# Optimization experiments

Hardware: AMD Instinct MI355X
Metric: run time of the kernel (lower is better)

## Reference

```python
import jax, jax.numpy as jnp
import numpy as np

NUM_HEADS = 16
HIDDEN = 1024
HEAD_DIM = HIDDEN // NUM_HEADS


def setup_inputs() -> dict:
    key = jax.random.key(0)
    ks = jax.random.split(key, 9)
    B, S, D = 2, 2048, HIDDEN
    s = 1.0 / np.sqrt(D)
    return {
        "x": jax.random.normal(ks[0], (B, S, D), dtype=jnp.float32),
        "Wq": jax.random.normal(ks[1], (D, D), dtype=jnp.float32) * s,
        "bq": jnp.zeros((D,), dtype=jnp.float32),
        "Wk": jax.random.normal(ks[2], (D, D), dtype=jnp.float32) * s,
        "bk": jnp.zeros((D,), dtype=jnp.float32),
        "Wv": jax.random.normal(ks[3], (D, D), dtype=jnp.float32) * s,
        "bv": jnp.zeros((D,), dtype=jnp.float32),
        "Wo": jax.random.normal(ks[4], (D, D), dtype=jnp.float32) * s,
        "bo": jnp.zeros((D,), dtype=jnp.float32),
    }


def reference(x, Wq, bq, Wk, bk, Wv, bv, Wo, bo):
    B, S, D = x.shape
    H, Hd = NUM_HEADS, HEAD_DIM
    # projections -> [B, H, S, Hd]
    def proj(W, b):
        return (x @ W + b).reshape(B, S, H, Hd).transpose(0, 2, 1, 3)
    q = proj(Wq, bq)
    k = proj(Wk, bk)
    v = proj(Wv, bv)
    scores = jnp.einsum('bhqd,bhkd->bhqk', q, k) / jnp.sqrt(jnp.float32(Hd))
    p_attn = jax.nn.softmax(scores, axis=-1)  # dropout = identity (eval)
    ctx = jnp.einsum('bhqk,bhkd->bhqd', p_attn, v)
    attn_mean = jnp.mean(p_attn, axis=1)  # [B, S, S]
    out = ctx.transpose(0, 2, 1, 3).reshape(B, S, D) @ Wo + bo
    return out, attn_mean
```

## Files before the change

### kernel.cpp

```cpp
#include <hip/hip_runtime.h>
#include <math.h>

#define NUM_HEADS 16
#define HEAD_DIM  64
#define HIDDEN    1024
#define BATCH     2
#define SEQ       2048

#define QSCALE 0.1803368801111204f

typedef short bf16x8 __attribute__((ext_vector_type(8)));
typedef short short4v __attribute__((ext_vector_type(4)));
typedef float f32x4 __attribute__((ext_vector_type(4)));

#if __has_builtin(__builtin_amdgcn_exp2f)
#define EXP2F __builtin_amdgcn_exp2f
#else
#define EXP2F exp2f
#endif

#define ACQB(N) do { asm volatile("s_waitcnt vmcnt(" #N ")" ::: "memory"); \
                     __builtin_amdgcn_s_barrier(); } while (0)
#define RELB()  do { asm volatile("s_waitcnt lgkmcnt(0)" ::: "memory");   \
                     __builtin_amdgcn_sched_barrier(0);                    \
                     __builtin_amdgcn_s_barrier(); } while (0)
#define BARR()  do { asm volatile("s_waitcnt vmcnt(0) lgkmcnt(0)" ::: "memory"); \
                     __builtin_amdgcn_sched_barrier(0);                    \
                     __builtin_amdgcn_s_barrier(); } while (0)

__device__ __forceinline__ short f2bf(float f) {
    union { float f; unsigned int u; } x; x.f = f;
    unsigned int r = x.u + 0x7fffu + ((x.u >> 16) & 1u);
    return (short)(r >> 16);
}

__device__ __forceinline__ unsigned int pack_bf16_trunc(float lo, float hi) {
    return __builtin_amdgcn_perm(__float_as_uint(hi), __float_as_uint(lo), 0x07060302u);
}

__device__ __forceinline__ void async16(const void* g, void* l) {
    __builtin_amdgcn_global_load_lds(
        (const __attribute__((address_space(1))) void*)g,
        (__attribute__((address_space(3))) void*)l, 16, 0, 0);
}

__global__ __launch_bounds__(256)
void prep_kernel(const float* __restrict__ x,
                 const float* __restrict__ Wq, const float* __restrict__ Wk,
                 const float* __restrict__ Wv, const float* __restrict__ Wo,
                 short* __restrict__ xb, short* __restrict__ Wt4)
{
    __shared__ float t[64][65];
    const int tid = threadIdx.x;
    const int bid = blockIdx.x;
    if (bid < 4096) {
        size_t i = ((size_t)bid * 256 + tid) * 4;
        float4 v = *(const float4*)&x[i];
        short4v o;
        o.x = f2bf(v.x); o.y = f2bf(v.y); o.z = f2bf(v.z); o.w = f2bf(v.w);
        *(short4v*)&xb[i] = o;
        return;
    }
    const int tb = bid - 4096;
    const int z  = tb >> 8;
    const int cx = tb & 15, cy = (tb >> 4) & 15;
    const float* W = (z == 0) ? Wq : (z == 1) ? Wk : (z == 2) ? Wv : Wo;
    short* dst = Wt4 + (size_t)z * HIDDEN * HIDDEN;
    const int c0 = cx * 64;
    const int r0 = cy * 64;
    const int cl = tid & 63, rw = tid >> 6;
    #pragma unroll
    for (int p = 0; p < 16; ++p) {
        int row = p * 4 + rw;
        t[row][cl] = W[(size_t)(r0 + row) * HIDDEN + c0 + cl];
    }
    __syncthreads();
    #pragma unroll
    for (int p = 0; p < 16; ++p) {
        int orow = p * 4 + rw;
        dst[(size_t)(c0 + orow) * HIDDEN + r0 + cl] = f2bf(t[cl][orow]);
    }
}

__global__ __launch_bounds__(256)
void qkv_proj_kernel(const short* __restrict__ xb, const short* __restrict__ Wt4,
                     const float* __restrict__ bq, const float* __restrict__ bk,
                     const float* __restrict__ bv,
                     short* __restrict__ Qb, short* __restrict__ Kb,
                     short* __restrict__ Vt)
{
    __shared__ short ldsA[128 * 64];
    __shared__ short ldsB[128 * 64];
    const int tid = threadIdx.x;
    const int lane = tid & 63, w = tid >> 6;
    const int l = lane & 15, q = lane >> 4;
    const int lin = blockIdx.y * 8 + blockIdx.x;
    const int cid = (lin & 7) * 32 + (lin >> 3);
    const int n0 = (cid & 7) * 128;
    const int m0 = (cid >> 3) * 128;
    const int z  = blockIdx.z;
    const short* Wt = Wt4 + (size_t)z * HIDDEN * HIDDEN;
    const int wm = (w >> 1) * 64, wn = (w & 1) * 64;
    const int sw = l & 7;

    const short* pa[4]; const short* pb[4]; int ldst[4];
    #pragma unroll
    for (int hh = 0; hh < 4; ++hh) {
        int c = hh * 256 + tid;
        int row = c >> 3;
        int kcg = (c & 7) ^ (row & 7);
        pa[hh] = xb + (size_t)(m0 + row) * HIDDEN + kcg * 8;
        pb[hh] = Wt + (size_t)(n0 + row) * HIDDEN + kcg * 8;
        ldst[hh] = c * 8;
    }

    f32x4 acc[4][4];
    #pragma unroll
    for (int i = 0; i < 4; ++i)
        #pragma unroll
        for (int j = 0; j < 4; ++j)
            acc[i][j] = (f32x4){0.f, 0.f, 0.f, 0.f};

    auto STG = [&]() {
        #pragma unroll
        for (int hh = 0; hh < 4; ++hh) {
            async16(pa[hh], &ldsA[ldst[hh]]);
            async16(pb[hh], &ldsB[ldst[hh]]);
            pa[hh] += 64; pb[hh] += 64;
        }
    };

    STG();
    ACQB(0);
    for (int t = 0; t < 16; ++t) {
        bf16x8 af[4][2], bfr[4][2];
        #pragma unroll
        for (int kk = 0; kk < 2; ++kk) {
            const int cc = ((4 * kk + q) ^ sw) * 8;
            #pragma unroll
            for (int i = 0; i < 4; ++i)
                af[i][kk] = *(const bf16x8*)&ldsA[(wm + 16 * i + l) * 64 + cc];
            #pragma unroll
            for (int j = 0; j < 4; ++j)
                bfr[j][kk] = *(const bf16x8*)&ldsB[(wn + 16 * j + l) * 64 + cc];
        }
        RELB();
        if (t < 15) STG();
        __builtin_amdgcn_s_setprio(1);
        #pragma unroll
        for (int kk = 0; kk < 2; ++kk)
            #pragma unroll
            for (int i = 0; i < 4; ++i)
                #pragma unroll
                for (int j = 0; j < 4; ++j)
                    acc[i][j] = __builtin_amdgcn_mfma_f32_16x16x32_bf16(
                        af[i][kk], bfr[j][kk], acc[i][j], 0, 0, 0);
        __builtin_amdgcn_s_setprio(0);
        if (t < 15) ACQB(0);
    }

    const float* bias = (z == 0) ? bq : (z == 1) ? bk : bv;
    const float sc = (z == 0) ? QSCALE : 1.0f;
    if (z < 2) {
        short* Ob = (z == 0) ? Qb : Kb;
        #pragma unroll
        for (int j = 0; j < 4; ++j) {
            int n = n0 + wn + 16 * j + l;
            float bval = bias[n];
            int h = n >> 6, hd = n & 63;
            #pragma unroll
            for (int i = 0; i < 4; ++i) {
                #pragma unroll
                for (int reg = 0; reg < 4; ++reg) {
                    int m = m0 + wm + 16 * i + 4 * q + reg;
                    int b_ = m >> 11, s = m & 2047;
                    Ob[(((size_t)(b_ * NUM_HEADS + h) * SEQ) + s) * HEAD_DIM + hd] =
                        f2bf((acc[i][j][reg] + bval) * sc);
                }
            }
        }
    } else {
        #pragma unroll
        for (int j = 0; j < 4; ++j) {
            int n = n0 + wn + 16 * j + l;
            float bval = bias[n];
            int h = n >> 6, hd = n & 63;
            #pragma unroll
            for (int i = 0; i < 4; ++i) {
                int mb = m0 + wm + 16 * i + 4 * q;
                int b_ = mb >> 11, s = mb & 2047;
                short4v pk;
                #pragma unroll
                for (int reg = 0; reg < 4; ++reg)
                    pk[reg] = f2bf(acc[i][j][reg] + bval);
                *(short4v*)&Vt[(((size_t)(b_ * NUM_HEADS + h) * HEAD_DIM) + hd) * SEQ + s] = pk;
            }
        }
    }
}

__global__ __launch_bounds__(512, 4)
void flash_kernel(const short* __restrict__ Qb, const short* __restrict__ Kb,
                  const short* __restrict__ Vt, short* __restrict__ Cb,
                  float* __restrict__ Lb)
{
    __shared__ __align__(16) char fsm[35840];
    short (*Ks)[64 * 64] = (short (*)[64 * 64])fsm;
    short (*Vs)[64 * 64] = (short (*)[64 * 64])(fsm + 16384);
    float (*Xch)[64][35] = (float (*)[64][35])fsm;

    const int tid = threadIdx.x, lane = tid & 63, w = tid >> 6;
    const int l = lane & 15, q = lane >> 4;
    const int qg = w & 3;
    const int kh = w >> 2;
    const int q0 = blockIdx.x * 128;
    const int Q0 = q0 + qg * 32;
    const int h = blockIdx.y, b = blockIdx.z;
    const size_t base  = (size_t)(b * NUM_HEADS + h) * SEQ * HEAD_DIM;
    const size_t vbase = (size_t)(b * NUM_HEADS + h) * HEAD_DIM * SEQ;

    bf16x8 bq[2][2];
    #pragma unroll
    for (int u = 0; u < 2; ++u)
        #pragma unroll
        for (int ks = 0; ks < 2; ++ks)
            bq[u][ks] = *(const bf16x8*)(Qb + base +
                (size_t)(Q0 + 16 * u + l) * HEAD_DIM + 32 * ks + 8 * q);

    const int c = tid;
    const int row = c >> 3;
    const int g = ((c & 7) ^ (row & 7)) * 8;
    const short* kp = Kb + base + (size_t)row * HEAD_DIM + g;
    const short* vp = Vt + vbase + (size_t)row * SEQ + g;

    const int sw = l & 7;
    int kaddr[2];
    #pragma unroll
    for (int ks = 0; ks < 2; ++ks)
        kaddr[ks] = (32 * kh + l) * 64 + ((4 * ks + q) ^ sw) * 8;
    const int vc0 = 4 * kh + (q >> 1);
    const int vaddr0 = l * 64 + ((vc0      ^ sw) * 8) + 4 * (q & 1);
    const int vaddr1 = l * 64 + (((vc0 + 2) ^ sw) * 8) + 4 * (q & 1);

    f32x4 ctx[2][4];
    #pragma unroll
    for (int u = 0; u < 2; ++u)
        #pragma unroll
        for (int m = 0; m < 4; ++m) ctx[u][m] = (f32x4){0.f, 0.f, 0.f, 0.f};
    float l_part[2] = {0.f, 0.f};

    auto STG = [&](int buf) {
        async16(kp, &Ks[buf][c * 8]);
        async16(vp, &Vs[buf][c * 8]);
        kp += 64 * HEAD_DIM;
        vp += 64;
    };
    auto CMP = [&](int buf) {
        f32x4 st[2][2];
        #pragma unroll
        for (int u = 0; u < 2; ++u)
            #pragma unroll
            for (int t = 0; t < 2; ++t) st[u][t] = (f32x4){0.f, 0.f, 0.f, 0.f};
        __builtin_amdgcn_s_setprio(1);
        #pragma unroll
        for (int ks = 0; ks < 2; ++ks) {
            #pragma unroll
            for (int t = 0; t < 2; ++t) {
                bf16x8 ak = *(const bf16x8*)&Ks[buf][kaddr[ks] + t * 1024];
                st[0][t] = __builtin_amdgcn_mfma_f32_16x16x32_bf16(ak, bq[0][ks], st[0][t], 0, 0, 0);
                st[1][t] = __builtin_amdgcn_mfma_f32_16x16x32_bf16(ak, bq[1][ks], st[1][t], 0, 0, 0);
            }
        }
        __builtin_amdgcn_s_setprio(0);
        union { unsigned int u32[4]; bf16x8 v; } bp[2];
        #pragma unroll
        for (int u = 0; u < 2; ++u) {
            #pragma unroll
            for (int t = 0; t < 2; ++t) {
                float p0 = EXP2F(st[u][t][0]);
                float p1 = EXP2F(st[u][t][1]);
                float p2 = EXP2F(st[u][t][2]);
                float p3 = EXP2F(st[u][t][3]);
                l_part[u] += (p0 + p1) + (p2 + p3);
                bp[u].u32[2 * t]     = pack_bf16_trunc(p0, p1);
                bp[u].u32[2 * t + 1] = pack_bf16_trunc(p2, p3);
            }
        }
        __builtin_amdgcn_s_setprio(1);
        #pragma unroll
        for (int m = 0; m < 4; ++m) {
            short4v g0 = *(const short4v*)&Vs[buf][vaddr0 + m * 1024];
            short4v g1 = *(const short4v*)&Vs[buf][vaddr1 + m * 1024];
            bf16x8 av = __builtin_shufflevector(g0, g1, 0, 1, 2, 3, 4, 5, 6, 7);
            ctx[0][m] = __builtin_amdgcn_mfma_f32_16x16x32_bf16(av, bp[0].v, ctx[0][m], 0, 0, 0);
            ctx[1][m] = __builtin_amdgcn_mfma_f32_16x16x32_bf16(av, bp[1].v, ctx[1][m], 0, 0, 0);
        }
        __builtin_amdgcn_s_setprio(0);
    };

    STG(0);
    for (int t = 0; t < 32; ++t) {
        BARR();
        if (t < 31) STG((t + 1) & 1);
        CMP(t & 1);
    }

    __syncthreads();

    if (kh == 1) {
        float* dst = &Xch[qg][lane][0];
        #pragma unroll
        for (int u = 0; u < 2; ++u)
            #pragma unroll
            for (int m = 0; m < 4; ++m)
                #pragma unroll
                for (int r = 0; r < 4; ++r)
                    dst[u * 16 + m * 4 + r] = ctx[u][m][r];
        dst[32] = l_part[0];
        dst[33] = l_part[1];
    }
    __syncthreads();
    if (kh == 0) {
        const float* src = &Xch[qg][lane][0];
        #pragma unroll
        for (int u = 0; u < 2; ++u)
            #pragma unroll
            for (int m = 0; m < 4; ++m)
                #pragma unroll
                for (int r = 0; r < 4; ++r)
                    ctx[u][m][r] += src[u * 16 + m * 4 + r];

        #pragma unroll
        for (int u = 0; u < 2; ++u) {
            float rs = l_part[u] + src[32 + u];
            rs += __shfl_xor(rs, 16);
            rs += __shfl_xor(rs, 32);
            float inv_l = 1.0f / rs;
            int s = Q0 + 16 * u + l;
            #pragma unroll
            for (int t = 0; t < 4; ++t) {
                short4v pk;
                #pragma unroll
                for (int reg = 0; reg < 4; ++reg)
                    pk[reg] = f2bf(ctx[u][t][reg] * inv_l);
                *(short4v*)&Cb[(((size_t)(b * NUM_HEADS + h) * SEQ) + s) * HEAD_DIM + 16 * t + 4 * q] = pk;
            }
            if (q == 0)
                Lb[(size_t)(b * NUM_HEADS + h) * SEQ + s] = inv_l;
        }
    }
}

__global__ __launch_bounds__(256)
void tail_kernel(const short* __restrict__ Cb, const short* __restrict__ Wot,
                 const float* __restrict__ bo, float* __restrict__ out,
                 const short* __restrict__ Qb, const short* __restrict__ Kb,
                 const float* __restrict__ Lb, float* __restrict__ amean)
{
    __shared__ __align__(16) short smem[26624];
    const int tid = threadIdx.x, lane = tid & 63, w = tid >> 6;
    const int l = lane & 15, q = lane >> 4;
    const int sw = l & 7;
    const int bid = blockIdx.x;
    const int r3 = bid % 3, g3 = bid / 3;

    if (r3 == 2) {
        short (*ldsA)[64 * 64]  = (short (*)[64 * 64])smem;
        short (*ldsB)[128 * 64] = (short (*)[128 * 64])(smem + 8192);
        const int cid = (g3 & 7) * 64 + (g3 >> 3);
        const int n0 = (cid & 7) * 128;
        const int m0 = (cid >> 3) * 64;

        const short* pa[2]; const short* pb[4]; int lda[2], ldb[4];
        #pragma unroll
        for (int hh = 0; hh < 2; ++hh) {
            int cc = hh * 256 + tid;
            int rowc = cc >> 3;
            int kcg = (cc & 7) ^ (rowc & 7);
            int m = m0 + rowc;
            int b_ = m >> 11, s = m & 2047;
            pa[hh] = Cb + (((size_t)(b_ * NUM_HEADS) * SEQ) + s) * HEAD_DIM + kcg * 8;
            lda[hh] = cc * 8;
        }
        #pragma unroll
        for (int hh = 0; hh < 4; ++hh) {
            int cc = hh * 256 + tid;
            int rowc = cc >> 3;
            int kcg = (cc & 7) ^ (rowc & 7);
            pb[hh] = Wot + (size_t)(n0 + rowc) * HIDDEN + kcg * 8;
            ldb[hh] = cc * 8;
        }

        f32x4 acc[4][2];
        #pragma unroll
        for (int i = 0; i < 4; ++i)
            #pragma unroll
            for (int jj = 0; jj < 2; ++jj)
                acc[i][jj] = (f32x4){0.f, 0.f, 0.f, 0.f};

        auto STG = [&](int buf) {
            #pragma unroll
            for (int hh = 0; hh < 2; ++hh) {
                async16(pa[hh], &ldsA[buf][lda[hh]]);
                pa[hh] += (size_t)SEQ * HEAD_DIM;
            }
            #pragma unroll
            for (int hh = 0; hh < 4; ++hh) {
                async16(pb[hh], &ldsB[buf][ldb[hh]]);
                pb[hh] += 64;
            }
        };
        auto CMP = [&](int buf) {
            #pragma unroll
            for (int kk = 0; kk < 2; ++kk) {
                const int cc = ((4 * kk + q) ^ sw) * 8;
                bf16x8 af[4], bfr[2];
                #pragma unroll
                for (int i = 0; i < 4; ++i)
                    af[i] = *(const bf16x8*)&ldsA[buf][(16 * i + l) * 64 + cc];
                #pragma unroll
                for (int jj = 0; jj < 2; ++jj)
                    bfr[jj] = *(const bf16x8*)&ldsB[buf][(32 * w + 16 * jj + l) * 64 + cc];
                __builtin_amdgcn_s_setprio(1);
                #pragma unroll
                for (int i = 0; i < 4; ++i)
                    #pragma unroll
                    for (int jj = 0; jj < 2; ++jj)
                        acc[i][jj] = __builtin_amdgcn_mfma_f32_16x16x32_bf16(
                            af[i], bfr[jj], acc[i][jj], 0, 0, 0);
                __builtin_amdgcn_s_setprio(0);
            }
        };

        STG(0);
        for (int t = 0; t < 16; ++t) {
            BARR();
            if (t < 15) STG((t + 1) & 1);
            CMP(t & 1);
        }

        #pragma unroll
        for (int jj = 0; jj < 2; ++jj) {
            int n = n0 + 32 * w + 16 * jj + l;
            float bval = bo[n];
            #pragma unroll
            for (int i = 0; i < 4; ++i)
                #pragma unroll
                for (int reg = 0; reg < 4; ++reg) {
                    int m = m0 + 16 * i + 4 * q + reg;
                    out[(size_t)m * HIDDEN + n] = acc[i][jj][reg] + bval;
                }
        }
    } else {
        short (*Qs)[64 * 64]  = (short (*)[64 * 64])smem;
        short (*Ks)[128 * 64] = (short (*)[128 * 64])(smem + 8192);
        float* Ls = (float*)(smem + 24576);
        const int a  = g3 * 2 + r3;
        const int k0 = (a & 15) * 128;
        const int qy = (a >> 4) & 31;
        const int q0 = qy * 64;
        const int b  = a >> 9;
        const size_t HSTRIDE = (size_t)SEQ * HEAD_DIM;

        const short* qp[2];
        const short* kp[4];
        {
            const size_t base0 = (size_t)(b * NUM_HEADS) * HSTRIDE;
            #pragma unroll
            for (int i = 0; i < 2; ++i) {
                int cc = 256 * i + tid;
                int rowc = cc >> 3;
                int gg = ((cc & 7) ^ (rowc & 7)) * 8;
                qp[i] = Qb + base0 + (size_t)(q0 + rowc) * HEAD_DIM + gg;
            }
            #pragma unroll
            for (int i = 0; i < 4; ++i) {
                int cc = 256 * i + tid;
                int rowc = cc >> 3;
                int gg = ((cc & 7) ^ (rowc & 7)) * 8;
                kp[i] = Kb + base0 + (size_t)(k0 + rowc) * HEAD_DIM + gg;
            }
        }

        f32x4 macc[2][4];
        #pragma unroll
        for (int tk = 0; tk < 2; ++tk)
            #pragma unroll
            for (int tq = 0; tq < 4; ++tq)
                macc[tk][tq] = (f32x4){0.f, 0.f, 0.f, 0.f};

        auto STG = [&](int buf) {
            #pragma unroll
            for (int i = 0; i < 2; ++i) { async16(qp[i], &Qs[buf][(256 * i + tid) * 8]); qp[i] += HSTRIDE; }
            #pragma unroll
            for (int i = 0; i < 4; ++i) { async16(kp[i], &Ks[buf][(256 * i + tid) * 8]); kp[i] += HSTRIDE; }
        };
        int hc = 0;
        auto CMP = [&](int buf) {
            int h = hc++;
            float linv[4];
            #pragma unroll
            for (int tq = 0; tq < 4; ++tq)
                linv[tq] = Ls[h * 64 + 16 * tq + l];

            bf16x8 bq[4][2], ak[2][2];
            #pragma unroll
            for (int ks = 0; ks < 2; ++ks) {
                const int cc = ((4 * ks + q) ^ sw) * 8;
                #pragma unroll
                for (int tq = 0; tq < 4; ++tq)
                    bq[tq][ks] = *(const bf16x8*)&Qs[buf][(16 * tq + l) * 64 + cc];
                #pragma unroll
                for (int tk = 0; tk < 2; ++tk)
                    ak[tk][ks] = *(const bf16x8*)&Ks[buf][(32 * w + 16 * tk + l) * 64 + cc];
            }
            #pragma unroll
            for (int tk = 0; tk < 2; ++tk) {
                #pragma unroll
                for (int tq = 0; tq < 4; ++tq) {
                    f32x4 st = (f32x4){0.f, 0.f, 0.f, 0.f};
                    st = __builtin_amdgcn_mfma_f32_16x16x32_bf16(ak[tk][0], bq[tq][0], st, 0, 0, 0);
                    st = __builtin_amdgcn_mfma_f32_16x16x32_bf16(ak[tk][1], bq[tq][1], st, 0, 0, 0);
                    float li = linv[tq];
                    #pragma unroll
                    for (int reg = 0; reg < 4; ++reg)
                        macc[tk][tq][reg] += EXP2F(st[reg]) * li;
                }
            }
        };

        {
            int hh = tid >> 4, cc = tid & 15;
            async16(Lb + ((size_t)(b * NUM_HEADS) + hh) * SEQ + q0 + cc * 4,
                    &Ls[hh * 64 + cc * 4]);
        }
        STG(0);
        for (int t = 0; t < 16; ++t) {
            BARR();
            if (t < 15) STG((t + 1) & 1);
            CMP(t & 1);
        }

        const float inv_h = 1.0f / (float)NUM_HEADS;
        #pragma unroll
        for (int tq = 0; tq < 4; ++tq) {
            int row_q = q0 + 16 * tq + l;
            #pragma unroll
            for (int tk = 0; tk < 2; ++tk) {
                int col_k = k0 + 32 * w + 16 * tk + 4 * q;
                f32x4 o;
                #pragma unroll
                for (int reg = 0; reg < 4; ++reg) o[reg] = macc[tk][tq][reg] * inv_h;
                *(f32x4*)&amean[((size_t)b * SEQ + row_q) * SEQ + col_k] = o;
            }
        }
    }
}

extern "C" void kernel_launch(void* const* d_in, const int* in_sizes, int n_in,
                              void* d_out, int out_size, void* d_ws, size_t ws_size,
                              hipStream_t stream)
{
    const float* x  = (const float*)d_in[0];
    const float* Wq = (const float*)d_in[1];
    const float* bq = (const float*)d_in[2];
    const float* Wk = (const float*)d_in[3];
    const float* bk = (const float*)d_in[4];
    const float* Wv = (const float*)d_in[5];
    const float* bv = (const float*)d_in[6];
    const float* Wo = (const float*)d_in[7];
    const float* bo = (const float*)d_in[8];

    float* out   = (float*)d_out;
    float* amean = out + (size_t)BATCH * SEQ * HIDDEN;

    const size_t NELEM = (size_t)BATCH * NUM_HEADS * SEQ * HEAD_DIM;
    short* ws  = (short*)d_ws;
    short* xb  = ws;
    short* Wt4 = xb + NELEM;
    short* Qb  = Wt4 + 4 * (size_t)HIDDEN * HIDDEN;
    short* Kb  = Qb + NELEM;
    short* Vt  = Kb + NELEM;
    short* Cb  = Vt + NELEM;
    float* Lb  = (float*)(Cb + NELEM);

    dim3 blk(256);
    prep_kernel<<<dim3(4096 + 1024), blk, 0, stream>>>(x, Wq, Wk, Wv, Wo, xb, Wt4);
    qkv_proj_kernel<<<dim3(8, 32, 3), blk, 0, stream>>>(xb, Wt4, bq, bk, bv, Qb, Kb, Vt);
    flash_kernel<<<dim3(SEQ / 128, NUM_HEADS, BATCH), dim3(512), 0, stream>>>(Qb, Kb, Vt, Cb, Lb);
    tail_kernel<<<dim3(1536), blk, 0, stream>>>(Cb, Wt4 + 3 * (size_t)HIDDEN * HIDDEN, bo, out,
                                                Qb, Kb, Lb, amean);
}
```

Baseline: 218.5 us.

## Double-buffer QKV/out-proj K-tiles at depth 32 and load Q directly to registers

The QKV projection moves from a single 64-wide K buffer with acquire/release barriers to a double-buffered 32-wide K pipeline using a 4-way XOR swizzle. The output projection in the tail kernel gets the same narrower double-buffered tiling. In the attention-mean path, Q fragments are now loaded straight from global memory into registers instead of being staged through LDS, and the warp tiling changes to 64 keys by 32 queries per wave. Together these cut LDS use and are meant to improve occupancy and load/compute overlap, at the cost of twice as many barrier iterations and uncached direct global loads of Q.

```diff
diff --git a/kernel.cpp b/kernel.cpp
--- a/kernel.cpp
+++ b/kernel.cpp
@@ -19,11 +19,6 @@
 #define EXP2F exp2f
 #endif
 
-#define ACQB(N) do { asm volatile("s_waitcnt vmcnt(" #N ")" ::: "memory"); \
-                     __builtin_amdgcn_s_barrier(); } while (0)
-#define RELB()  do { asm volatile("s_waitcnt lgkmcnt(0)" ::: "memory");   \
-                     __builtin_amdgcn_sched_barrier(0);                    \
-                     __builtin_amdgcn_s_barrier(); } while (0)
 #define BARR()  do { asm volatile("s_waitcnt vmcnt(0) lgkmcnt(0)" ::: "memory"); \
                      __builtin_amdgcn_sched_barrier(0);                    \
                      __builtin_amdgcn_s_barrier(); } while (0)
@@ -89,8 +84,8 @@
                      short* __restrict__ Qb, short* __restrict__ Kb,
                      short* __restrict__ Vt)
 {
-    __shared__ short ldsA[128 * 64];
-    __shared__ short ldsB[128 * 64];
+    __shared__ short ldsA[2][128 * 32];
+    __shared__ short ldsB[2][128 * 32];
     const int tid = threadIdx.x;
     const int lane = tid & 63, w = tid >> 6;
     const int l = lane & 15, q = lane >> 4;
@@ -101,14 +96,14 @@
     const int z  = blockIdx.z;
     const short* Wt = Wt4 + (size_t)z * HIDDEN * HIDDEN;
     const int wm = (w >> 1) * 64, wn = (w & 1) * 64;
-    const int sw = l & 7;
-
-    const short* pa[4]; const short* pb[4]; int ldst[4];
-    #pragma unroll
-    for (int hh = 0; hh < 4; ++hh) {
+    const int sw2 = (l >> 1) & 3;
+
+    const short* pa[2]; const short* pb[2]; int ldst[2];
+    #pragma unroll
+    for (int hh = 0; hh < 2; ++hh) {
         int c = hh * 256 + tid;
-        int row = c >> 3;
-        int kcg = (c & 7) ^ (row & 7);
+        int row = c >> 2;
+        int kcg = (c & 3) ^ ((c >> 3) & 3);
         pa[hh] = xb + (size_t)(m0 + row) * HIDDEN + kcg * 8;
         pb[hh] = Wt + (size_t)(n0 + row) * HIDDEN + kcg * 8;
         ldst[hh] = c * 8;
@@ -121,42 +116,38 @@
         for (int j = 0; j < 4; ++j)
             acc[i][j] = (f32x4){0.f, 0.f, 0.f, 0.f};
 
-    auto STG = [&]() {
-        #pragma unroll
-        for (int hh = 0; hh < 4; ++hh) {
-            async16(pa[hh], &ldsA[ldst[hh]]);
-            async16(pb[hh], &ldsB[ldst[hh]]);
-            pa[hh] += 64; pb[hh] += 64;
+    auto STG = [&](int buf) {
+        #pragma unroll
+        for (int hh = 0; hh < 2; ++hh) {
+            async16(pa[hh], &ldsA[buf][ldst[hh]]);
+            async16(pb[hh], &ldsB[buf][ldst[hh]]);
+            pa[hh] += 32; pb[hh] += 32;
         }
     };
-
-    STG();
-    ACQB(0);
-    for (int t = 0; t < 16; ++t) {
-        bf16x8 af[4][2], bfr[4][2];
-        #pragma unroll
-        for (int kk = 0; kk < 2; ++kk) {
-            const int cc = ((4 * kk + q) ^ sw) * 8;
-            #pragma unroll
-            for (int i = 0; i < 4; ++i)
-                af[i][kk] = *(const bf16x8*)&ldsA[(wm + 16 * i + l) * 64 + cc];
+    auto CMP = [&](int buf) {
+        const int cc = (q ^ sw2) * 8;
+        bf16x8 af[4], bfr[4];
+        #pragma unroll
+        for (int i = 0; i < 4; ++i)
+            af[i] = *(const bf16x8*)&ldsA[buf][(wm + 16 * i + l) * 32 + cc];
+        #pragma unroll
+        for (int j = 0; j < 4; ++j)
+            bfr[j] = *(const bf16x8*)&ldsB[buf][(wn + 16 * j + l) * 32 + cc];
+        __builtin_amdgcn_s_setprio(1);
+        #pragma unroll
+        for (int i = 0; i < 4; ++i)
             #pragma unroll
             for (int j = 0; j < 4; ++j)
-                bfr[j][kk] = *(const bf16x8*)&ldsB[(wn + 16 * j + l) * 64 + cc];
-        }
-        RELB();
-        if (t < 15) STG();
-        __builtin_amdgcn_s_setprio(1);
-        #pragma unroll
-        for (int kk = 0; kk < 2; ++kk)
-            #pragma unroll
-            for (int i = 0; i < 4; ++i)
-                #pragma unroll
-                for (int j = 0; j < 4; ++j)
-                    acc[i][j] = __builtin_amdgcn_mfma_f32_16x16x32_bf16(
-                        af[i][kk], bfr[j][kk], acc[i][j], 0, 0, 0);
+                acc[i][j] = __builtin_amdgcn_mfma_f32_16x16x32_bf16(
+                    af[i], bfr[j], acc[i][j], 0, 0, 0);
         __builtin_amdgcn_s_setprio(0);
-        if (t < 15) ACQB(0);
+    };
+
+    STG(0);
+    for (int t = 0; t < 32; ++t) {
+        BARR();
+        if (t < 31) STG((t + 1) & 1);
+        CMP(t & 1);
     }
 
     const float* bias = (z == 0) ? bq : (z == 1) ? bk : bv;
@@ -357,36 +348,36 @@
                  const short* __restrict__ Qb, const short* __restrict__ Kb,
                  const float* __restrict__ Lb, float* __restrict__ amean)
 {
-    __shared__ __align__(16) short smem[26624];
+    __shared__ __align__(16) short smem[18432];
     const int tid = threadIdx.x, lane = tid & 63, w = tid >> 6;
     const int l = lane & 15, q = lane >> 4;
-    const int sw = l & 7;
     const int bid = blockIdx.x;
     const int r3 = bid % 3, g3 = bid / 3;
 
     if (r3 == 2) {
-        short (*ldsA)[64 * 64]  = (short (*)[64 * 64])smem;
-        short (*ldsB)[128 * 64] = (short (*)[128 * 64])(smem + 8192);
+        short (*ldsA)[64 * 32]  = (short (*)[64 * 32])smem;
+        short (*ldsB)[128 * 32] = (short (*)[128 * 32])(smem + 4096);
         const int cid = (g3 & 7) * 64 + (g3 >> 3);
         const int n0 = (cid & 7) * 128;
         const int m0 = (cid >> 3) * 64;
-
-        const short* pa[2]; const short* pb[4]; int lda[2], ldb[4];
+        const int sw2 = (l >> 1) & 3;
+        const size_t HSTRIDE = (size_t)SEQ * HEAD_DIM;
+
+        const short* pa; const short* pb[2]; int lda, ldb[2];
+        {
+            int cc = tid;
+            int rowc = cc >> 2;
+            int kcg = (cc & 3) ^ ((cc >> 3) & 3);
+            int m = m0 + rowc;
+            int b_ = m >> 11, s = m & 2047;
+            pa = Cb + (((size_t)(b_ * NUM_HEADS) * SEQ) + s) * HEAD_DIM + kcg * 8;
+            lda = cc * 8;
+        }
         #pragma unroll
         for (int hh = 0; hh < 2; ++hh) {
             int cc = hh * 256 + tid;
-            int rowc = cc >> 3;
-            int kcg = (cc & 7) ^ (rowc & 7);
-            int m = m0 + rowc;
-            int b_ = m >> 11, s = m & 2047;
-            pa[hh] = Cb + (((size_t)(b_ * NUM_HEADS) * SEQ) + s) * HEAD_DIM + kcg * 8;
-            lda[hh] = cc * 8;
-        }
-        #pragma unroll
-        for (int hh = 0; hh < 4; ++hh) {
-            int cc = hh * 256 + tid;
-            int rowc = cc >> 3;
-            int kcg = (cc & 7) ^ (rowc & 7);
+            int rowc = cc >> 2;
+            int kcg = (cc & 3) ^ ((cc >> 3) & 3);
             pb[hh] = Wot + (size_t)(n0 + rowc) * HIDDEN + kcg * 8;
             ldb[hh] = cc * 8;
         }
@@ -398,44 +389,40 @@
             for (int jj = 0; jj < 2; ++jj)
                 acc[i][jj] = (f32x4){0.f, 0.f, 0.f, 0.f};
 
+        int stg_t = 0;
         auto STG = [&](int buf) {
+            async16(pa, &ldsA[buf][lda]);
+            pa += (stg_t & 1) ? (HSTRIDE - 32) : 32;
+            ++stg_t;
             #pragma unroll
             for (int hh = 0; hh < 2; ++hh) {
-                async16(pa[hh], &ldsA[buf][lda[hh]]);
-                pa[hh] += (size_t)SEQ * HEAD_DIM;
-            }
-            #pragma unroll
-            for (int hh = 0; hh < 4; ++hh) {
                 async16(pb[hh], &ldsB[buf][ldb[hh]]);
-                pb[hh] += 64;
+                pb[hh] += 32;
             }
         };
         auto CMP = [&](int buf) {
-            #pragma unroll
-            for (int kk = 0; kk < 2; ++kk) {
-                const int cc = ((4 * kk + q) ^ sw) * 8;
-                bf16x8 af[4], bfr[2];
-                #pragma unroll
-                for (int i = 0; i < 4; ++i)
-                    af[i] = *(const bf16x8*)&ldsA[buf][(16 * i + l) * 64 + cc];
+            const int cc = (q ^ sw2) * 8;
+            bf16x8 af[4], bfr[2];
+            #pragma unroll
+            for (int i = 0; i < 4; ++i)
+                af[i] = *(const bf16x8*)&ldsA[buf][(16 * i + l) * 32 + cc];
+            #pragma unroll
+            for (int jj = 0; jj < 2; ++jj)
+                bfr[jj] = *(const bf16x8*)&ldsB[buf][(32 * w + 16 * jj + l) * 32 + cc];
+            __builtin_amdgcn_s_setprio(1);
+            #pragma unroll
+            for (int i = 0; i < 4; ++i)
                 #pragma unroll
                 for (int jj = 0; jj < 2; ++jj)
-                    bfr[jj] = *(const bf16x8*)&ldsB[buf][(32 * w + 16 * jj + l) * 64 + cc];
-                __builtin_amdgcn_s_setprio(1);
-                #pragma unroll
-                for (int i = 0; i < 4; ++i)
-                    #pragma unroll
-                    for (int jj = 0; jj < 2; ++jj)
-                        acc[i][jj] = __builtin_amdgcn_mfma_f32_16x16x32_bf16(
-                            af[i], bfr[jj], acc[i][jj], 0, 0, 0);
-                __builtin_amdgcn_s_setprio(0);
-            }
+                    acc[i][jj] = __builtin_amdgcn_mfma_f32_16x16x32_bf16(
+                        af[i], bfr[jj], acc[i][jj], 0, 0, 0);
+            __builtin_amdgcn_s_setprio(0);
         };
 
         STG(0);
-        for (int t = 0; t < 16; ++t) {
+        for (int t = 0; t < 32; ++t) {
             BARR();
-            if (t < 15) STG((t + 1) & 1);
+            if (t < 31) STG((t + 1) & 1);
             CMP(t & 1);
         }
 
@@ -452,72 +439,75 @@
                 }
         }
     } else {
-        short (*Qs)[64 * 64]  = (short (*)[64 * 64])smem;
-        short (*Ks)[128 * 64] = (short (*)[128 * 64])(smem + 8192);
-        float* Ls = (float*)(smem + 24576);
+        short (*Ks)[128 * 64] = (short (*)[128 * 64])smem;
+        float* Ls = (float*)(smem + 16384);
         const int a  = g3 * 2 + r3;
         const int k0 = (a & 15) * 128;
         const int qy = (a >> 4) & 31;
         const int q0 = qy * 64;
         const int b  = a >> 9;
+        const int wk0 = (w & 1) * 64, wq0 = (w >> 1) * 32;
+        const int sw = l & 7;
         const size_t HSTRIDE = (size_t)SEQ * HEAD_DIM;
-
-        const short* qp[2];
+        const size_t base0 = (size_t)(b * NUM_HEADS) * HSTRIDE;
+
         const short* kp[4];
-        {
-            const size_t base0 = (size_t)(b * NUM_HEADS) * HSTRIDE;
-            #pragma unroll
-            for (int i = 0; i < 2; ++i) {
-                int cc = 256 * i + tid;
-                int rowc = cc >> 3;
-                int gg = ((cc & 7) ^ (rowc & 7)) * 8;
-                qp[i] = Qb + base0 + (size_t)(q0 + rowc) * HEAD_DIM + gg;
-            }
-            #pragma unroll
-            for (int i = 0; i < 4; ++i) {
-                int cc = 256 * i + tid;
-                int rowc = cc >> 3;
-                int gg = ((cc & 7) ^ (rowc & 7)) * 8;
-                kp[i] = Kb + base0 + (size_t)(k0 + rowc) * HEAD_DIM + gg;
-            }
-        }
-
-        f32x4 macc[2][4];
-        #pragma unroll
-        for (int tk = 0; tk < 2; ++tk)
-            #pragma unroll
-            for (int tq = 0; tq < 4; ++tq)
+        #pragma unroll
+        for (int i = 0; i < 4; ++i) {
+            int cc = 256 * i + tid;
+            int rowc = cc >> 3;
+            int gg = ((cc & 7) ^ (rowc & 7)) * 8;
+            kp[i] = Kb + base0 + (size_t)(k0 + rowc) * HEAD_DIM + gg;
+        }
+        const short* qbase = Qb + base0 + (size_t)(q0 + wq0 + l) * HEAD_DIM + 8 * q;
+
+        f32x4 macc[4][2];
+        #pragma unroll
+        for (int tk = 0; tk < 4; ++tk)
+            #pragma unroll
+            for (int tq = 0; tq < 2; ++tq)
                 macc[tk][tq] = (f32x4){0.f, 0.f, 0.f, 0.f};
 
         auto STG = [&](int buf) {
-            #pragma unroll
-            for (int i = 0; i < 2; ++i) { async16(qp[i], &Qs[buf][(256 * i + tid) * 8]); qp[i] += HSTRIDE; }
             #pragma unroll
             for (int i = 0; i < 4; ++i) { async16(kp[i], &Ks[buf][(256 * i + tid) * 8]); kp[i] += HSTRIDE; }
         };
-        int hc = 0;
-        auto CMP = [&](int buf) {
-            int h = hc++;
-            float linv[4];
-            #pragma unroll
-            for (int tq = 0; tq < 4; ++tq)
-                linv[tq] = Ls[h * 64 + 16 * tq + l];
-
-            bf16x8 bq[4][2], ak[2][2];
+
+        {
+            int hh = tid >> 4, cc = tid & 15;
+            async16(Lb + ((size_t)(b * NUM_HEADS) + hh) * SEQ + q0 + cc * 4,
+                    &Ls[hh * 64 + cc * 4]);
+        }
+        STG(0);
+        for (int t = 0; t < 16; ++t) {
+            BARR();
+            bf16x8 bq[2][2];
+            #pragma unroll
+            for (int tq = 0; tq < 2; ++tq)
+                #pragma unroll
+                for (int ks = 0; ks < 2; ++ks)
+                    bq[tq][ks] = *(const bf16x8*)(qbase + (size_t)t * HSTRIDE +
+                                                  tq * 16 * HEAD_DIM + 32 * ks);
+            __builtin_amdgcn_sched_barrier(0);
+            if (t < 15) STG((t + 1) & 1);
+
+            float linv[2];
+            #pragma unroll
+            for (int tq = 0; tq < 2; ++tq)
+                linv[tq] = Ls[t * 64 + wq0 + 16 * tq + l];
+
+            bf16x8 ak[4][2];
             #pragma unroll
             for (int ks = 0; ks < 2; ++ks) {
                 const int cc = ((4 * ks + q) ^ sw) * 8;
                 #pragma unroll
-                for (int tq = 0; tq < 4; ++tq)
-                    bq[tq][ks] = *(const bf16x8*)&Qs[buf][(16 * tq + l) * 64 + cc];
-                #pragma unroll
-                for (int tk = 0; tk < 2; ++tk)
-                    ak[tk][ks] = *(const bf16x8*)&Ks[buf][(32 * w + 16 * tk + l) * 64 + cc];
-            }
-            #pragma unroll
-            for (int tk = 0; tk < 2; ++tk) {
-                #pragma unroll
-                for (int tq = 0; tq < 4; ++tq) {
+                for (int tk = 0; tk < 4; ++tk)
+                    ak[tk][ks] = *(const bf16x8*)&Ks[t & 1][(wk0 + 16 * tk + l) * 64 + cc];
+            }
+            #pragma unroll
+            for (int tk = 0; tk < 4; ++tk) {
+                #pragma unroll
+                for (int tq = 0; tq < 2; ++tq) {
                     f32x4 st = (f32x4){0.f, 0.f, 0.f, 0.f};
                     st = __builtin_amdgcn_mfma_f32_16x16x32_bf16(ak[tk][0], bq[tq][0], st, 0, 0, 0);
                     st = __builtin_amdgcn_mfma_f32_16x16x32_bf16(ak[tk][1], bq[tq][1], st, 0, 0, 0);
@@ -527,27 +517,15 @@
                         macc[tk][tq][reg] += EXP2F(st[reg]) * li;
                 }
             }
-        };
-
-        {
-            int hh = tid >> 4, cc = tid & 15;
-            async16(Lb + ((size_t)(b * NUM_HEADS) + hh) * SEQ + q0 + cc * 4,
-                    &Ls[hh * 64 + cc * 4]);
-        }
-        STG(0);
-        for (int t = 0; t < 16; ++t) {
-            BARR();
-            if (t < 15) STG((t + 1) & 1);
-            CMP(t & 1);
         }
 
         const float inv_h = 1.0f / (float)NUM_HEADS;
         #pragma unroll
-        for (int tq = 0; tq < 4; ++tq) {
-            int row_q = q0 + 16 * tq + l;
-            #pragma unroll
-            for (int tk = 0; tk < 2; ++tk) {
-                int col_k = k0 + 32 * w + 16 * tk + 4 * q;
+        for (int tq = 0; tq < 2; ++tq) {
+            int row_q = q0 + wq0 + 16 * tq + l;
+            #pragma unroll
+            for (int tk = 0; tk < 4; ++tk) {
+                int col_k = k0 + wk0 + 16 * tk + 4 * q;
                 f32x4 o;
                 #pragma unroll
                 for (int reg = 0; reg < 4; ++reg) o[reg] = macc[tk][tq][reg] * inv_h;
```

New measurement: 253.0 us. +15.8%, slower.
